# Kernel tuning notes

Measured on AMD Instinct MI355X. Metric: run time of the kernel, lower is better.

## Reference

```python
import jax, jax.numpy as jnp
import numpy as np

EPS = 1e-6

def _complex_linear(xr, xi, wr, wi):
    # torch Linear: y = x @ W.T ; complex: (xr+i*xi)(Wr+i*Wi)
    yr = jnp.einsum('bsd,ed->bse', xr, wr) - jnp.einsum('bsd,ed->bse', xi, wi)
    yi = jnp.einsum('bsd,ed->bse', xr, wi) + jnp.einsum('bsd,ed->bse', xi, wr)
    return yr, yi

def setup_inputs() -> dict:
    key = jax.random.key(0)
    ks = jax.random.split(key, 12)
    B, S, D = 32768, 16, 64
    inp = {
        'z_real': jax.random.normal(ks[0], (B, D), jnp.float32),
        'z_imag': jax.random.normal(ks[1], (B, D), jnp.float32),
        'mem':    jax.random.normal(ks[2], (B, S, 2 * D), jnp.float32),
        'ptr':    jax.random.uniform(ks[3], (B, S), jnp.float32),
        'ctrl':   jax.random.normal(ks[4], (B, 3), jnp.float32),
        'wq_r': jax.random.normal(ks[5], (D, D), jnp.float32) / np.sqrt(D),
        'wq_i': jax.random.normal(ks[6], (D, D), jnp.float32) / np.sqrt(D),
        'wk_r': jax.random.normal(ks[7], (D, D), jnp.float32) / np.sqrt(D),
        'wk_i': jax.random.normal(ks[8], (D, D), jnp.float32) / np.sqrt(D),
        'wv_r': jax.random.normal(ks[9], (D, D), jnp.float32) / np.sqrt(D),
        'wv_i': jax.random.normal(ks[10], (D, D), jnp.float32) / np.sqrt(D),
    }
    return inp

def reference(z_real, z_imag, mem, ptr, ctrl, wq_r, wq_i, wk_r, wk_i, wv_r, wv_i):
    D = z_real.shape[-1]
    # soft push/pop/stay gates, normalized
    g = jax.nn.sigmoid(ctrl)  # (B,3)
    push, pop, stay = g[:, 0:1], g[:, 1:2], g[:, 2:3]
    total = push + pop + stay + EPS
    push, pop, stay = push / total, pop / total, stay / total
    # pointer update via rolls
    ptr_up = jnp.roll(ptr, 1, axis=1)
    ptr_down = jnp.roll(ptr, -1, axis=1)
    new_ptr = push * ptr_up + pop * ptr_down + stay * ptr  # (B,S)
    # memory write
    z_flat = jnp.concatenate([z_real, z_imag], axis=-1)  # (B,2D)
    mem_new = mem * (1.0 - push[..., None]) + push[..., None] * z_flat[:, None, :]
    mr, mi = mem_new[..., :D], mem_new[..., D:]  # (B,S,D) complex memory
    # complex attention over stack slots
    qr, qi = _complex_linear(mr, mi, wq_r, wq_i)
    kr, ki = _complex_linear(mr, mi, wk_r, wk_i)
    vr, vi = _complex_linear(mr, mi, wv_r, wv_i)
    q_flat = jnp.concatenate([qr, qi], axis=-1)  # (B,S,2D)
    k_flat = jnp.concatenate([kr, ki], axis=-1)
    scale = D ** (-0.5)
    scores = jnp.einsum('bse,bte->bst', q_flat, k_flat) * scale  # (B,S,S)
    attn = jax.nn.softmax(scores, axis=-1)
    ar = jnp.einsum('bst,btd->bsd', attn, vr)
    ai = jnp.einsum('bst,btd->bsd', attn, vi)
    att_flat = jnp.concatenate([ar, ai], axis=-1)  # (B,S,2D)
    # pointer-weighted read
    read_flat = (att_flat * new_ptr[..., None]).sum(axis=1)  # (B,2D)
    z_read_r, z_read_i = read_flat[:, :D], read_flat[:, D:]
    active_slots = (new_ptr > 0.1).astype(jnp.float32).sum(axis=1).mean()
    return (z_read_r, z_read_i, mem_new, new_ptr, active_slots)
```

## Files before the change

### kernel.cpp

```cpp
#include <hip/hip_runtime.h>


typedef __bf16 bf16x8 __attribute__((ext_vector_type(8)));
typedef float  f32x4  __attribute__((ext_vector_type(4)));

#define B_TOT   32768
#define GRID_WG 512
#define NWAVES  4096
#define BPW     8

__device__ __forceinline__ unsigned short f2bf(float x) {
  __bf16 h = (__bf16)x;
  return __builtin_bit_cast(unsigned short, h);
}
__device__ __forceinline__ float sigm(float x) { return 1.0f / (1.0f + expf(-x)); }

__global__ void ems_zero(unsigned int* c) { if (threadIdx.x == 0) *c = 0u; }

__global__ void ems_fin(const unsigned int* __restrict__ c, float* __restrict__ out) {
  if (threadIdx.x == 0) out[0] = (float)(*c) * (1.0f / 32768.0f);
}

__global__ void __launch_bounds__(128)
ems_mt(const float* __restrict__ wqr, const float* __restrict__ wqi,
       const float* __restrict__ wkr, const float* __restrict__ wki,
       unsigned short* __restrict__ mt)
{
  __shared__ float sK[128];
  const int e2 = (int)blockIdx.x;
  const int e  = (int)threadIdx.x;
  float kv;
  if (e < 64) kv = (e2 < 64) ? wkr[e*64 + e2]      : -wki[e*64 + (e2-64)];
  else        kv = (e2 < 64) ? wki[(e-64)*64 + e2] :  wkr[(e-64)*64 + (e2-64)];
  sK[e] = kv;
  __syncthreads();
  float acc = 0.0f;
  #pragma unroll 8
  for (int Ep = 0; Ep < 64; ++Ep) {
    float q = (e < 64) ? wqr[Ep*64 + e] : -wqi[Ep*64 + (e-64)];
    acc += q * sK[Ep];
  }
  #pragma unroll 8
  for (int Ep = 0; Ep < 64; ++Ep) {
    float q = (e < 64) ? wqi[Ep*64 + e] : wqr[Ep*64 + (e-64)];
    acc += q * sK[64 + Ep];
  }
  mt[e2*128 + e] = f2bf(acc);
}

__global__ void __launch_bounds__(512, 4)
ems_main(const float* __restrict__ z_real, const float* __restrict__ z_imag,
         const float* __restrict__ mem,    const float* __restrict__ ptrv,
         const float* __restrict__ ctrl,
         const float* __restrict__ wvr,    const float* __restrict__ wvi,
         const unsigned short* __restrict__ mt,
         float* __restrict__ out_zr, float* __restrict__ out_zi,
         float* __restrict__ out_mem, float* __restrict__ out_ptr,
         unsigned int* __restrict__ ws_cnt)
{
  __shared__ __align__(16) unsigned short lds[40960];

  const int tid = (int)threadIdx.x;

  for (int idx = tid; idx < 16384; idx += 512) {
    int e2 = idx >> 7, e = idx & 127;
    lds[(e2 << 7) + ((((e >> 3) ^ (e2 & 15))) << 3) + (e & 7)] = mt[idx];
  }
  #pragma unroll
  for (int m = 0; m < 2; ++m) {
    const float* wp = m ? wvi : wvr;
    for (int idx = tid; idx < 4096; idx += 512) {
      int e = idx >> 6, d = idx & 63;
      lds[16384 + (m << 12) + (e << 6) + (((d >> 3) ^ (e & 7)) << 3) + (d & 7)] = f2bf(wp[idx]);
    }
  }
  __syncthreads();

  const int lane = tid & 63;
  const int wv   = tid >> 6;
  const int c    = lane & 15;
  const int g    = lane >> 4;

  unsigned short* SY = &lds[24576 + (wv << 11)];

  const float4* mem4 = (const float4*)mem;
  const float4* zr4  = (const float4*)z_real;
  const float4* zi4  = (const float4*)z_imag;
  float4* omem4 = (float4*)out_mem;

  unsigned int active_acc = 0u;
  const int b0 = (int)blockIdx.x * 8 + wv;

  for (int it = 0; it < BPW; ++it) {
    const int b = b0 + it * NWAVES;

    float4 cm[8], cz[8];
    #pragma unroll
    for (int t4 = 0; t4 < 4; ++t4) {
      int i4 = b*512 + c*32 + t4*8 + g*2;
      cm[2*t4]   = mem4[i4];
      cm[2*t4+1] = mem4[i4+1];
    }
    {
      int zb = b*16 + g*2;
      cz[0] = zr4[zb];   cz[1] = zr4[zb+1];
      cz[2] = zr4[zb+8]; cz[3] = zr4[zb+9];
      cz[4] = zi4[zb];   cz[5] = zi4[zb+1];
      cz[6] = zi4[zb+8]; cz[7] = zi4[zb+9];
    }

    float pu = sigm(ctrl[b*3+0]);
    float po = sigm(ctrl[b*3+1]);
    float st = sigm(ctrl[b*3+2]);
    float tot = pu + po + st + 1e-6f;
    pu /= tot; po /= tot; st /= tot;

    float pm = ptrv[b*16 + ((c+15)&15)];
    float pp = ptrv[b*16 + ((c+ 1)&15)];
    float pc = ptrv[b*16 + c];
    float np = pu*pm + po*pp + st*pc;
    if (g == 0) out_ptr[b*16 + c] = np;
    unsigned long long ball = __ballot(np > 0.1f);
    active_acc += (unsigned int)__popcll(ball & 0xFFFFull);

    float omp = 1.0f - pu;
    bf16x8 af[4], afn[2];
    #pragma unroll
    for (int t4 = 0; t4 < 4; ++t4) {
      float4 a0 = cm[2*t4], a1 = cm[2*t4+1];
      float4 z0 = cz[2*t4], z1 = cz[2*t4+1];
      float4 r0, r1;
      r0.x = a0.x*omp + pu*z0.x;  r0.y = a0.y*omp + pu*z0.y;
      r0.z = a0.z*omp + pu*z0.z;  r0.w = a0.w*omp + pu*z0.w;
      r1.x = a1.x*omp + pu*z1.x;  r1.y = a1.y*omp + pu*z1.y;
      r1.z = a1.z*omp + pu*z1.z;  r1.w = a1.w*omp + pu*z1.w;
      int i4 = b*512 + c*32 + t4*8 + g*2;
      omem4[i4]   = r0;
      omem4[i4+1] = r1;
      af[t4][0]=(__bf16)r0.x; af[t4][1]=(__bf16)r0.y; af[t4][2]=(__bf16)r0.z; af[t4][3]=(__bf16)r0.w;
      af[t4][4]=(__bf16)r1.x; af[t4][5]=(__bf16)r1.y; af[t4][6]=(__bf16)r1.z; af[t4][7]=(__bf16)r1.w;
      if (t4 >= 2) {
        afn[t4-2][0]=(__bf16)(-r0.x); afn[t4-2][1]=(__bf16)(-r0.y);
        afn[t4-2][2]=(__bf16)(-r0.z); afn[t4-2][3]=(__bf16)(-r0.w);
        afn[t4-2][4]=(__bf16)(-r1.x); afn[t4-2][5]=(__bf16)(-r1.y);
        afn[t4-2][6]=(__bf16)(-r1.z); afn[t4-2][7]=(__bf16)(-r1.w);
      }
    }

    #pragma unroll
    for (int n2 = 0; n2 < 8; ++n2) {
      int e2 = (n2 << 4) + c;
      f32x4 acc = {0.f,0.f,0.f,0.f};
      #pragma unroll
      for (int t = 0; t < 4; ++t) {
        bf16x8 bm = *(const bf16x8*)&lds[(e2 << 7) + ((((t << 2) + g) ^ c) << 3)];
        acc = __builtin_amdgcn_mfma_f32_16x16x32_bf16(af[t], bm, acc, 0, 0, 0);
      }
      int chb = (n2 << 1) | (c >> 3);
      #pragma unroll
      for (int i = 0; i < 4; ++i) {
        int s = (g << 2) + i;
        SY[(s << 7) + ((chb ^ s) << 3) + (c & 7)] = f2bf(acc[i]);
      }
    }

    f32x4 sc = {0.f,0.f,0.f,0.f};
    #pragma unroll
    for (int t = 0; t < 4; ++t) {
      bf16x8 aq = *(const bf16x8*)&SY[(c << 7) + ((((t << 2) + g) ^ c) << 3)];
      sc = __builtin_amdgcn_mfma_f32_16x16x32_bf16(aq, af[t], sc, 0, 0, 0);
    }
    float a4[4];
    #pragma unroll
    for (int i = 0; i < 4; ++i) {
      float s0 = sc[i] * 0.125f;
      float mx = s0;
      mx = fmaxf(mx, __shfl_xor(mx, 1, 64));
      mx = fmaxf(mx, __shfl_xor(mx, 2, 64));
      mx = fmaxf(mx, __shfl_xor(mx, 4, 64));
      mx = fmaxf(mx, __shfl_xor(mx, 8, 64));
      float ex = expf(s0 - mx);
      float sm = ex;
      sm += __shfl_xor(sm, 1, 64);
      sm += __shfl_xor(sm, 2, 64);
      sm += __shfl_xor(sm, 4, 64);
      sm += __shfl_xor(sm, 8, 64);
      a4[i] = ex / sm;
    }

    float npi[4];
    #pragma unroll
    for (int i = 0; i < 4; ++i) npi[i] = __shfl(np, (g << 2) + i, 64);
    float pw = a4[0]*npi[0] + a4[1]*npi[1] + a4[2]*npi[2] + a4[3]*npi[3];
    pw += __shfl_xor(pw, 16, 64);
    pw += __shfl_xor(pw, 32, 64);
    float w4[4];
    #pragma unroll
    for (int i = 0; i < 4; ++i) w4[i] = __shfl(pw, (g << 2) + i, 64);

    #pragma unroll
    for (int n = 0; n < 4; ++n) {
      int e = (n << 4) + c, e7 = e & 7, eb = 16384 + (e << 6);
      f32x4 ar = {0.f,0.f,0.f,0.f}, ai = {0.f,0.f,0.f,0.f};
      #pragma unroll
      for (int t = 0; t < 2; ++t) {
        int ch = (((t << 2) + g) ^ e7) << 3;
        bf16x8 fr = *(const bf16x8*)&lds[eb + ch];
        bf16x8 fi = *(const bf16x8*)&lds[eb + 4096 + ch];
        ar = __builtin_amdgcn_mfma_f32_16x16x32_bf16(af[t],   fr, ar, 0,0,0);
        ai = __builtin_amdgcn_mfma_f32_16x16x32_bf16(af[t],   fi, ai, 0,0,0);
        ar = __builtin_amdgcn_mfma_f32_16x16x32_bf16(afn[t],  fi, ar, 0,0,0);
        ai = __builtin_amdgcn_mfma_f32_16x16x32_bf16(af[t+2], fr, ai, 0,0,0);
      }
      float prr = ar[0]*w4[0] + ar[1]*w4[1] + ar[2]*w4[2] + ar[3]*w4[3];
      float pri = ai[0]*w4[0] + ai[1]*w4[1] + ai[2]*w4[2] + ai[3]*w4[3];
      prr += __shfl_xor(prr, 16, 64);
      prr += __shfl_xor(prr, 32, 64);
      pri += __shfl_xor(pri, 16, 64);
      pri += __shfl_xor(pri, 32, 64);
      if (g == 0) {
        out_zr[b*64 + (n << 4) + c] = prr;
        out_zi[b*64 + (n << 4) + c] = pri;
      }
    }
  }

  if (lane == 0) atomicAdd(ws_cnt, active_acc);
}

extern "C" void kernel_launch(void* const* d_in, const int* in_sizes, int n_in,
                              void* d_out, int out_size, void* d_ws, size_t ws_size,
                              hipStream_t stream) {
  const float* z_real = (const float*)d_in[0];
  const float* z_imag = (const float*)d_in[1];
  const float* memp   = (const float*)d_in[2];
  const float* ptrv   = (const float*)d_in[3];
  const float* ctrl   = (const float*)d_in[4];
  const float* wq_r   = (const float*)d_in[5];
  const float* wq_i   = (const float*)d_in[6];
  const float* wk_r   = (const float*)d_in[7];
  const float* wk_i   = (const float*)d_in[8];
  const float* wv_r   = (const float*)d_in[9];
  const float* wv_i   = (const float*)d_in[10];

  float* out     = (float*)d_out;
  float* out_zr  = out;
  float* out_zi  = out + 2097152;
  float* out_mem = out + 4194304;
  float* out_ptr = out + 71303168;
  float* out_sc  = out + 71827456;

  unsigned int*   cnt = (unsigned int*)d_ws;
  unsigned short* mt  = (unsigned short*)((char*)d_ws + 1024);

  ems_zero<<<1, 64, 0, stream>>>(cnt);
  ems_mt<<<128, 128, 0, stream>>>(wq_r, wq_i, wk_r, wk_i, mt);
  ems_main<<<GRID_WG, 512, 0, stream>>>(z_real, z_imag, memp, ptrv, ctrl,
                                        wv_r, wv_i, mt,
                                        out_zr, out_zi, out_mem, out_ptr, cnt);
  ems_fin<<<1, 64, 0, stream>>>(cnt, out_sc);
}
```

Baseline: 180.6 us.

## Software-pipeline batch loads and process two batches per wave iteration

Restructures the main loop so each wave handles two batch elements per iteration and prefetches the next pair's mem/z/ptr/ctrl while running the MFMA chain on the current pair, hiding global load latency. It also stores mem_new nontemporally, replaces expf and division with exp2/rcp intrinsics, reorganizes the softmax-pointer weighting to drop the max subtraction, and folds the counter-zeroing kernel into the mt kernel. Register pressure rises a lot (launch bounds drop to 2 waves per SIMD and LDS use grows), and skipping the max subtraction risks overflow for large scores.

```diff
diff --git a/kernel.cpp b/kernel.cpp
--- a/kernel.cpp
+++ b/kernel.cpp
@@ -3,19 +3,20 @@
 
 typedef __bf16 bf16x8 __attribute__((ext_vector_type(8)));
 typedef float  f32x4  __attribute__((ext_vector_type(4)));
+typedef float  f4     __attribute__((ext_vector_type(4)));
 
 #define B_TOT   32768
 #define GRID_WG 512
 #define NWAVES  4096
-#define BPW     8
+#define LOG2E   1.4426950408889634f
 
 __device__ __forceinline__ unsigned short f2bf(float x) {
   __bf16 h = (__bf16)x;
   return __builtin_bit_cast(unsigned short, h);
 }
-__device__ __forceinline__ float sigm(float x) { return 1.0f / (1.0f + expf(-x)); }
-
-__global__ void ems_zero(unsigned int* c) { if (threadIdx.x == 0) *c = 0u; }
+__device__ __forceinline__ float rcp_f(float x) { return __builtin_amdgcn_rcpf(x); }
+__device__ __forceinline__ float ex2_f(float x) { return __builtin_amdgcn_exp2f(x); }
+__device__ __forceinline__ float sigm(float x) { return rcp_f(1.0f + ex2_f(-LOG2E * x)); }
 
 __global__ void ems_fin(const unsigned int* __restrict__ c, float* __restrict__ out) {
   if (threadIdx.x == 0) out[0] = (float)(*c) * (1.0f / 32768.0f);
@@ -24,8 +25,9 @@
 __global__ void __launch_bounds__(128)
 ems_mt(const float* __restrict__ wqr, const float* __restrict__ wqi,
        const float* __restrict__ wkr, const float* __restrict__ wki,
-       unsigned short* __restrict__ mt)
+       unsigned short* __restrict__ mt, unsigned int* __restrict__ cnt)
 {
+  if (blockIdx.x == 0 && threadIdx.x == 0) *cnt = 0u;
   __shared__ float sK[128];
   const int e2 = (int)blockIdx.x;
   const int e  = (int)threadIdx.x;
@@ -48,7 +50,7 @@
   mt[e2*128 + e] = f2bf(acc);
 }
 
-__global__ void __launch_bounds__(512, 4)
+__global__ void __launch_bounds__(512, 2)
 ems_main(const float* __restrict__ z_real, const float* __restrict__ z_imag,
          const float* __restrict__ mem,    const float* __restrict__ ptrv,
          const float* __restrict__ ctrl,
@@ -58,13 +60,13 @@
          float* __restrict__ out_mem, float* __restrict__ out_ptr,
          unsigned int* __restrict__ ws_cnt)
 {
-  __shared__ __align__(16) unsigned short lds[40960];
+  __shared__ __align__(16) unsigned short lds[57344];
 
   const int tid = (int)threadIdx.x;
 
   for (int idx = tid; idx < 16384; idx += 512) {
     int e2 = idx >> 7, e = idx & 127;
-    lds[(e2 << 7) + ((((e >> 3) ^ (e2 & 15))) << 3) + (e & 7)] = mt[idx];
+    lds[(e2 << 7) + (((e >> 3) ^ (e2 & 15)) << 3) + (e & 7)] = mt[idx];
   }
   #pragma unroll
   for (int m = 0; m < 2; ++m) {
@@ -81,148 +83,186 @@
   const int c    = lane & 15;
   const int g    = lane >> 4;
 
-  unsigned short* SY = &lds[24576 + (wv << 11)];
-
-  const float4* mem4 = (const float4*)mem;
-  const float4* zr4  = (const float4*)z_real;
-  const float4* zi4  = (const float4*)z_imag;
-  float4* omem4 = (float4*)out_mem;
+  unsigned short* SYp[2];
+  SYp[0] = &lds[24576 + (wv << 12)];
+  SYp[1] = SYp[0] + 2048;
+
+  const f4* mem4 = (const f4*)mem;
+  const f4* zr4  = (const f4*)z_real;
+  const f4* zi4  = (const f4*)z_imag;
+  f4* omem4 = (f4*)out_mem;
+
+  f4 cm[2][8], cz[2][8];
+  float pmv[2], ppv[2], pcv[2], ct0[2], ct1[2], ct2[2];
+
+  auto loadB = [&](int b, int q) {
+    #pragma unroll
+    for (int t4 = 0; t4 < 4; ++t4) {
+      int i4 = b*512 + c*32 + t4*8 + g*2;
+      cm[q][2*t4]   = mem4[i4];
+      cm[q][2*t4+1] = mem4[i4+1];
+    }
+    int zb = b*16 + g*2;
+    cz[q][0] = zr4[zb];   cz[q][1] = zr4[zb+1];
+    cz[q][2] = zr4[zb+8]; cz[q][3] = zr4[zb+9];
+    cz[q][4] = zi4[zb];   cz[q][5] = zi4[zb+1];
+    cz[q][6] = zi4[zb+8]; cz[q][7] = zi4[zb+9];
+    pmv[q] = ptrv[b*16 + ((c+15)&15)];
+    ppv[q] = ptrv[b*16 + ((c+ 1)&15)];
+    pcv[q] = ptrv[b*16 + c];
+    ct0[q] = ctrl[b*3+0]; ct1[q] = ctrl[b*3+1]; ct2[q] = ctrl[b*3+2];
+  };
 
   unsigned int active_acc = 0u;
   const int b0 = (int)blockIdx.x * 8 + wv;
-
-  for (int it = 0; it < BPW; ++it) {
-    const int b = b0 + it * NWAVES;
-
-    float4 cm[8], cz[8];
-    #pragma unroll
-    for (int t4 = 0; t4 < 4; ++t4) {
-      int i4 = b*512 + c*32 + t4*8 + g*2;
-      cm[2*t4]   = mem4[i4];
-      cm[2*t4+1] = mem4[i4+1];
-    }
-    {
-      int zb = b*16 + g*2;
-      cz[0] = zr4[zb];   cz[1] = zr4[zb+1];
-      cz[2] = zr4[zb+8]; cz[3] = zr4[zb+9];
-      cz[4] = zi4[zb];   cz[5] = zi4[zb+1];
-      cz[6] = zi4[zb+8]; cz[7] = zi4[zb+9];
-    }
-
-    float pu = sigm(ctrl[b*3+0]);
-    float po = sigm(ctrl[b*3+1]);
-    float st = sigm(ctrl[b*3+2]);
-    float tot = pu + po + st + 1e-6f;
-    pu /= tot; po /= tot; st /= tot;
-
-    float pm = ptrv[b*16 + ((c+15)&15)];
-    float pp = ptrv[b*16 + ((c+ 1)&15)];
-    float pc = ptrv[b*16 + c];
-    float np = pu*pm + po*pp + st*pc;
-    if (g == 0) out_ptr[b*16 + c] = np;
-    unsigned long long ball = __ballot(np > 0.1f);
-    active_acc += (unsigned int)__popcll(ball & 0xFFFFull);
-
-    float omp = 1.0f - pu;
-    bf16x8 af[4], afn[2];
-    #pragma unroll
-    for (int t4 = 0; t4 < 4; ++t4) {
-      float4 a0 = cm[2*t4], a1 = cm[2*t4+1];
-      float4 z0 = cz[2*t4], z1 = cz[2*t4+1];
-      float4 r0, r1;
-      r0.x = a0.x*omp + pu*z0.x;  r0.y = a0.y*omp + pu*z0.y;
-      r0.z = a0.z*omp + pu*z0.z;  r0.w = a0.w*omp + pu*z0.w;
-      r1.x = a1.x*omp + pu*z1.x;  r1.y = a1.y*omp + pu*z1.y;
-      r1.z = a1.z*omp + pu*z1.z;  r1.w = a1.w*omp + pu*z1.w;
-      int i4 = b*512 + c*32 + t4*8 + g*2;
-      omem4[i4]   = r0;
-      omem4[i4+1] = r1;
-      af[t4][0]=(__bf16)r0.x; af[t4][1]=(__bf16)r0.y; af[t4][2]=(__bf16)r0.z; af[t4][3]=(__bf16)r0.w;
-      af[t4][4]=(__bf16)r1.x; af[t4][5]=(__bf16)r1.y; af[t4][6]=(__bf16)r1.z; af[t4][7]=(__bf16)r1.w;
-      if (t4 >= 2) {
-        afn[t4-2][0]=(__bf16)(-r0.x); afn[t4-2][1]=(__bf16)(-r0.y);
-        afn[t4-2][2]=(__bf16)(-r0.z); afn[t4-2][3]=(__bf16)(-r0.w);
-        afn[t4-2][4]=(__bf16)(-r1.x); afn[t4-2][5]=(__bf16)(-r1.y);
-        afn[t4-2][6]=(__bf16)(-r1.z); afn[t4-2][7]=(__bf16)(-r1.w);
-      }
+  int bq[2];
+  bq[0] = b0;
+  bq[1] = b0 + NWAVES;
+  loadB(bq[0], 0);
+  loadB(bq[1], 1);
+
+  #pragma unroll 1
+  for (int p = 0; p < 4; ++p) {
+    int bcur[2] = { bq[0], bq[1] };
+
+    float npv[2], puv[2], ompv[2];
+    #pragma unroll
+    for (int q = 0; q < 2; ++q) {
+      float pu = sigm(ct0[q]);
+      float po = sigm(ct1[q]);
+      float st = sigm(ct2[q]);
+      float rt = rcp_f(pu + po + st + 1e-6f);
+      pu *= rt; po *= rt; st *= rt;
+      float np = pu*pmv[q] + po*ppv[q] + st*pcv[q];
+      if (g == 0) out_ptr[bcur[q]*16 + c] = np;
+      unsigned long long ball = __ballot(np > 0.1f);
+      active_acc += (unsigned int)__popcll(ball & 0xFFFFull);
+      npv[q] = np; puv[q] = pu; ompv[q] = 1.0f - pu;
+    }
+
+    bf16x8 af[2][4], afn[2][2];
+    #pragma unroll
+    for (int q = 0; q < 2; ++q) {
+      float pu = puv[q], om = ompv[q];
+      #pragma unroll
+      for (int t4 = 0; t4 < 4; ++t4) {
+        f4 r0 = cm[q][2*t4]   * om + pu * cz[q][2*t4];
+        f4 r1 = cm[q][2*t4+1] * om + pu * cz[q][2*t4+1];
+        int i4 = bcur[q]*512 + c*32 + t4*8 + g*2;
+        __builtin_nontemporal_store(r0, &omem4[i4]);
+        __builtin_nontemporal_store(r1, &omem4[i4+1]);
+        #pragma unroll
+        for (int k = 0; k < 4; ++k) {
+          af[q][t4][k]   = (__bf16)r0[k];
+          af[q][t4][4+k] = (__bf16)r1[k];
+        }
+        if (t4 >= 2) {
+          #pragma unroll
+          for (int k = 0; k < 4; ++k) {
+            afn[q][t4-2][k]   = (__bf16)(-r0[k]);
+            afn[q][t4-2][4+k] = (__bf16)(-r1[k]);
+          }
+        }
+      }
+    }
+
+    if (p < 3) {
+      loadB(bcur[0] + 2*NWAVES, 0);
+      loadB(bcur[1] + 2*NWAVES, 1);
     }
 
     #pragma unroll
     for (int n2 = 0; n2 < 8; ++n2) {
       int e2 = (n2 << 4) + c;
-      f32x4 acc = {0.f,0.f,0.f,0.f};
+      f32x4 acc0 = {0.f,0.f,0.f,0.f}, acc1 = {0.f,0.f,0.f,0.f};
       #pragma unroll
       for (int t = 0; t < 4; ++t) {
         bf16x8 bm = *(const bf16x8*)&lds[(e2 << 7) + ((((t << 2) + g) ^ c) << 3)];
-        acc = __builtin_amdgcn_mfma_f32_16x16x32_bf16(af[t], bm, acc, 0, 0, 0);
+        acc0 = __builtin_amdgcn_mfma_f32_16x16x32_bf16(af[0][t], bm, acc0, 0,0,0);
+        acc1 = __builtin_amdgcn_mfma_f32_16x16x32_bf16(af[1][t], bm, acc1, 0,0,0);
       }
       int chb = (n2 << 1) | (c >> 3);
       #pragma unroll
       for (int i = 0; i < 4; ++i) {
         int s = (g << 2) + i;
-        SY[(s << 7) + ((chb ^ s) << 3) + (c & 7)] = f2bf(acc[i]);
-      }
-    }
-
-    f32x4 sc = {0.f,0.f,0.f,0.f};
+        int off = (s << 7) + ((chb ^ s) << 3) + (c & 7);
+        SYp[0][off] = f2bf(acc0[i]);
+        SYp[1][off] = f2bf(acc1[i]);
+      }
+    }
+
+    f32x4 sc0 = {0.f,0.f,0.f,0.f}, sc1 = {0.f,0.f,0.f,0.f};
     #pragma unroll
     for (int t = 0; t < 4; ++t) {
-      bf16x8 aq = *(const bf16x8*)&SY[(c << 7) + ((((t << 2) + g) ^ c) << 3)];
-      sc = __builtin_amdgcn_mfma_f32_16x16x32_bf16(aq, af[t], sc, 0, 0, 0);
-    }
-    float a4[4];
-    #pragma unroll
-    for (int i = 0; i < 4; ++i) {
-      float s0 = sc[i] * 0.125f;
-      float mx = s0;
-      mx = fmaxf(mx, __shfl_xor(mx, 1, 64));
-      mx = fmaxf(mx, __shfl_xor(mx, 2, 64));
-      mx = fmaxf(mx, __shfl_xor(mx, 4, 64));
-      mx = fmaxf(mx, __shfl_xor(mx, 8, 64));
-      float ex = expf(s0 - mx);
-      float sm = ex;
-      sm += __shfl_xor(sm, 1, 64);
-      sm += __shfl_xor(sm, 2, 64);
-      sm += __shfl_xor(sm, 4, 64);
-      sm += __shfl_xor(sm, 8, 64);
-      a4[i] = ex / sm;
-    }
-
-    float npi[4];
-    #pragma unroll
-    for (int i = 0; i < 4; ++i) npi[i] = __shfl(np, (g << 2) + i, 64);
-    float pw = a4[0]*npi[0] + a4[1]*npi[1] + a4[2]*npi[2] + a4[3]*npi[3];
-    pw += __shfl_xor(pw, 16, 64);
-    pw += __shfl_xor(pw, 32, 64);
-    float w4[4];
-    #pragma unroll
-    for (int i = 0; i < 4; ++i) w4[i] = __shfl(pw, (g << 2) + i, 64);
+      int off = (c << 7) + ((((t << 2) + g) ^ c) << 3);
+      bf16x8 y0 = *(const bf16x8*)&SYp[0][off];
+      bf16x8 y1 = *(const bf16x8*)&SYp[1][off];
+      sc0 = __builtin_amdgcn_mfma_f32_16x16x32_bf16(af[0][t], y0, sc0, 0,0,0);
+      sc1 = __builtin_amdgcn_mfma_f32_16x16x32_bf16(af[1][t], y1, sc1, 0,0,0);
+    }
+
+    float w4[2][4];
+    #pragma unroll
+    for (int q = 0; q < 2; ++q) {
+      f32x4 scq = q ? sc1 : sc0;
+      float e0 = ex2_f(scq[0] * 0.18033688011112042f);
+      float e1 = ex2_f(scq[1] * 0.18033688011112042f);
+      float e2 = ex2_f(scq[2] * 0.18033688011112042f);
+      float e3 = ex2_f(scq[3] * 0.18033688011112042f);
+      float r = (e0 + e1) + (e2 + e3);
+      r += __shfl_xor(r, 16, 64);
+      r += __shfl_xor(r, 32, 64);
+      float u = npv[q] * rcp_f(r);
+      float v0 = u*e0, v1 = u*e1, v2 = u*e2, v3 = u*e3;
+      #pragma unroll
+      for (int d = 1; d <= 8; d <<= 1) {
+        v0 += __shfl_xor(v0, d, 64);
+        v1 += __shfl_xor(v1, d, 64);
+        v2 += __shfl_xor(v2, d, 64);
+        v3 += __shfl_xor(v3, d, 64);
+      }
+      w4[q][0] = v0; w4[q][1] = v1; w4[q][2] = v2; w4[q][3] = v3;
+    }
 
     #pragma unroll
     for (int n = 0; n < 4; ++n) {
-      int e = (n << 4) + c, e7 = e & 7, eb = 16384 + (e << 6);
-      f32x4 ar = {0.f,0.f,0.f,0.f}, ai = {0.f,0.f,0.f,0.f};
+      int eb = 16384 + (((n << 4) + c) << 6);
+      int e7 = c & 7;
+      f32x4 ar0 = {0.f,0.f,0.f,0.f}, ai0 = {0.f,0.f,0.f,0.f};
+      f32x4 ar1 = {0.f,0.f,0.f,0.f}, ai1 = {0.f,0.f,0.f,0.f};
       #pragma unroll
       for (int t = 0; t < 2; ++t) {
         int ch = (((t << 2) + g) ^ e7) << 3;
         bf16x8 fr = *(const bf16x8*)&lds[eb + ch];
         bf16x8 fi = *(const bf16x8*)&lds[eb + 4096 + ch];
-        ar = __builtin_amdgcn_mfma_f32_16x16x32_bf16(af[t],   fr, ar, 0,0,0);
-        ai = __builtin_amdgcn_mfma_f32_16x16x32_bf16(af[t],   fi, ai, 0,0,0);
-        ar = __builtin_amdgcn_mfma_f32_16x16x32_bf16(afn[t],  fi, ar, 0,0,0);
-        ai = __builtin_amdgcn_mfma_f32_16x16x32_bf16(af[t+2], fr, ai, 0,0,0);
-      }
-      float prr = ar[0]*w4[0] + ar[1]*w4[1] + ar[2]*w4[2] + ar[3]*w4[3];
-      float pri = ai[0]*w4[0] + ai[1]*w4[1] + ai[2]*w4[2] + ai[3]*w4[3];
-      prr += __shfl_xor(prr, 16, 64);
-      prr += __shfl_xor(prr, 32, 64);
-      pri += __shfl_xor(pri, 16, 64);
-      pri += __shfl_xor(pri, 32, 64);
-      if (g == 0) {
-        out_zr[b*64 + (n << 4) + c] = prr;
-        out_zi[b*64 + (n << 4) + c] = pri;
-      }
-    }
+        ar0 = __builtin_amdgcn_mfma_f32_16x16x32_bf16(af[0][t],   fr, ar0, 0,0,0);
+        ar1 = __builtin_amdgcn_mfma_f32_16x16x32_bf16(af[1][t],   fr, ar1, 0,0,0);
+        ai0 = __builtin_amdgcn_mfma_f32_16x16x32_bf16(af[0][t],   fi, ai0, 0,0,0);
+        ai1 = __builtin_amdgcn_mfma_f32_16x16x32_bf16(af[1][t],   fi, ai1, 0,0,0);
+        ar0 = __builtin_amdgcn_mfma_f32_16x16x32_bf16(afn[0][t],  fi, ar0, 0,0,0);
+        ar1 = __builtin_amdgcn_mfma_f32_16x16x32_bf16(afn[1][t],  fi, ar1, 0,0,0);
+        ai0 = __builtin_amdgcn_mfma_f32_16x16x32_bf16(af[0][t+2], fr, ai0, 0,0,0);
+        ai1 = __builtin_amdgcn_mfma_f32_16x16x32_bf16(af[1][t+2], fr, ai1, 0,0,0);
+      }
+      #pragma unroll
+      for (int q = 0; q < 2; ++q) {
+        f32x4 arq = q ? ar1 : ar0;
+        f32x4 aiq = q ? ai1 : ai0;
+        float prr = arq[0]*w4[q][0] + arq[1]*w4[q][1] + arq[2]*w4[q][2] + arq[3]*w4[q][3];
+        float pri = aiq[0]*w4[q][0] + aiq[1]*w4[q][1] + aiq[2]*w4[q][2] + aiq[3]*w4[q][3];
+        prr += __shfl_xor(prr, 16, 64);
+        prr += __shfl_xor(prr, 32, 64);
+        pri += __shfl_xor(pri, 16, 64);
+        pri += __shfl_xor(pri, 32, 64);
+        if (g == 0) {
+          out_zr[bcur[q]*64 + (n << 4) + c] = prr;
+          out_zi[bcur[q]*64 + (n << 4) + c] = pri;
+        }
+      }
+    }
+
+    bq[0] = bcur[0] + 2*NWAVES;
+    bq[1] = bcur[1] + 2*NWAVES;
   }
 
   if (lane == 0) atomicAdd(ws_cnt, active_acc);
@@ -253,8 +293,7 @@
   unsigned int*   cnt = (unsigned int*)d_ws;
   unsigned short* mt  = (unsigned short*)((char*)d_ws + 1024);
 
-  ems_zero<<<1, 64, 0, stream>>>(cnt);
-  ems_mt<<<128, 128, 0, stream>>>(wq_r, wq_i, wk_r, wk_i, mt);
+  ems_mt<<<128, 128, 0, stream>>>(wq_r, wq_i, wk_r, wk_i, mt, cnt);
   ems_main<<<GRID_WG, 512, 0, stream>>>(z_real, z_imag, memp, ptrv, ctrl,
                                         wv_r, wv_i, mt,
                                         out_zr, out_zi, out_mem, out_ptr, cnt);
```

Result: slower. 267.2 us (+48.0%).
